# Kernel optimization log

Hardware: AMD Instinct MI355X
Metric: run time of the kernel (lower is better)

The kernel has to match this reference:

```python
import jax, jax.numpy as jnp
import numpy as np

B, S, D, H = 4, 1024, 1024, 16
DH = D // H  # head_dim = 64


def setup_inputs() -> dict:
    key = jax.random.key(0)
    kq, kk, kv, kl, kwq, kwk, kwv, kwo = jax.random.split(key, 8)
    query = jax.random.normal(kq, (B, S, D), dtype=jnp.float32)
    key_t = jax.random.normal(kk, (B, S, D), dtype=jnp.float32)
    value = jax.random.normal(kv, (B, S, D), dtype=jnp.float32)
    # padding: keys at positions >= valid length are padded (True)
    lengths = jax.random.randint(kl, (B,), S // 2, S + 1)
    key_padding_mask = jnp.arange(S)[None, :] >= lengths[:, None]  # [B,S] bool
    scale = 1.0 / np.sqrt(D)
    Wq = jax.random.normal(kwq, (D, D), dtype=jnp.float32) * scale
    Wk = jax.random.normal(kwk, (D, D), dtype=jnp.float32) * scale
    Wv = jax.random.normal(kwv, (D, D), dtype=jnp.float32) * scale
    Wo = jax.random.normal(kwo, (D, D), dtype=jnp.float32) * scale
    gamma = jnp.ones((H,), dtype=jnp.float32)
    return {"query": query, "key": key_t, "value": value,
            "key_padding_mask": key_padding_mask,
            "Wq": Wq, "Wk": Wk, "Wv": Wv, "Wo": Wo, "gamma": gamma}


def reference(query, key, value, key_padding_mask, Wq, Wk, Wv, Wo, gamma):
    # nn.Linear(x) = x @ W.T (bias=False)
    q = jnp.einsum('bsd,ed->bse', query, Wq).reshape(B, S, H, DH).transpose(0, 2, 1, 3)  # [B,H,S,Dh]
    k = jnp.einsum('bsd,ed->bse', key, Wk).reshape(B, S, H, DH).transpose(0, 2, 1, 3)
    v = jnp.einsum('bsd,ed->bse', value, Wv).reshape(B, S, H, DH).transpose(0, 2, 1, 3)
    scores = jnp.einsum('bhqd,bhkd->bhqk', q, k) / jnp.sqrt(jnp.float32(DH))
    pad = key_padding_mask[:, None, None, :]  # [B,1,1,S]
    scores = jnp.where(pad, -jnp.inf, scores)
    v = jnp.where(key_padding_mask[:, None, :, None], 0.0, v)
    attn = jax.nn.softmax(scores, axis=-1)  # dropout p=0 (eval) -> identity
    ws = jnp.einsum('bhqk,bhkd->bhqd', attn, v)
    ws = ws * gamma[None, :, None, None]  # per-head scale
    ws = ws.transpose(0, 2, 1, 3).reshape(B, S, D)
    return jnp.einsum('bsd,ed->bse', ws, Wo)
```

## Files before the change

### kernel.cpp

```cpp
#include <hip/hip_runtime.h>
#include <math.h>

#define S_LEN 1024
#define DMODEL 1024

typedef __attribute__((ext_vector_type(8))) short bf16x8;
typedef __attribute__((ext_vector_type(4))) short bf16x4;
typedef __attribute__((ext_vector_type(4))) float f32x4;

#define MFMA16(a, b, c) __builtin_amdgcn_mfma_f32_16x16x32_bf16(a, b, c, 0, 0, 0)

#define WP (1024u * 1024u)
#define XP (4u * 1024u * 1024u)

__device__ __forceinline__ unsigned short rne_bf16(float f) {
    unsigned u = __float_as_uint(f);
    u += 0x7FFFu + ((u >> 16) & 1u);
    return (unsigned short)(u >> 16);
}

__device__ __forceinline__ void split_rne(float f, unsigned short& h, unsigned short& l) {
    unsigned short hh = rne_bf16(f);
    float lf = f - __uint_as_float(((unsigned)hh) << 16);
    h = hh;
    l = rne_bf16(lf);
}

typedef const __attribute__((address_space(1))) unsigned int* gas_t;
typedef __attribute__((address_space(3))) unsigned int* las_t;
__device__ __forceinline__ void glds16(const void* g, void* l) {
    __builtin_amdgcn_global_load_lds((gas_t)g, (las_t)l, 16, 0, 0);
}

__global__ __launch_bounds__(256)
void convert_wx(const float* __restrict__ W0, const float* __restrict__ W1,
                const float* __restrict__ W2, const float* __restrict__ W3,
                const float* __restrict__ Xq, const float* __restrict__ Xk,
                const float* __restrict__ Xv,
                unsigned short* __restrict__ Wpl, unsigned short* __restrict__ Xbase) {
    int blk = blockIdx.x;
    if (blk < 4096) {
        const int which = blk >> 10;
        const float* W = which == 0 ? W0 : which == 1 ? W1 : which == 2 ? W2 : W3;
        int i = ((blk & 1023) * 256 + threadIdx.x) * 4;
        float4 f = *(const float4*)&W[i];
        if (which == 3) {
            unsigned short* hi = Wpl + 3 * WP;
            unsigned short* lo = Wpl + 4 * WP;
            bf16x4 h, l;
            unsigned short hh, ll;
            split_rne(f.x, hh, ll); h[0] = (short)hh; l[0] = (short)ll;
            split_rne(f.y, hh, ll); h[1] = (short)hh; l[1] = (short)ll;
            split_rne(f.z, hh, ll); h[2] = (short)hh; l[2] = (short)ll;
            split_rne(f.w, hh, ll); h[3] = (short)hh; l[3] = (short)ll;
            *(bf16x4*)&hi[i] = h;
            *(bf16x4*)&lo[i] = l;
        } else {
            unsigned short* hi = Wpl + (size_t)which * WP;
            bf16x4 h;
            h[0] = (short)rne_bf16(f.x);
            h[1] = (short)rne_bf16(f.y);
            h[2] = (short)rne_bf16(f.z);
            h[3] = (short)rne_bf16(f.w);
            *(bf16x4*)&hi[i] = h;
        }
    } else {
        blk -= 4096;
        const int which = blk >> 12;
        const float* X = which == 0 ? Xq : which == 1 ? Xk : Xv;
        unsigned short* Xr = Xbase + (size_t)which * XP;
        int i = ((blk & 4095) * 256 + threadIdx.x) * 4;
        float4 f = *(const float4*)&X[i];
        bf16x4 h;
        h[0] = (short)rne_bf16(f.x);
        h[1] = (short)rne_bf16(f.y);
        h[2] = (short)rne_bf16(f.z);
        h[3] = (short)rne_bf16(f.w);
        *(bf16x4*)&Xr[i] = h;
    }
}

__global__ __launch_bounds__(256)
void gemm_proj(const unsigned short* __restrict__ Xbase,
               const unsigned short* __restrict__ Wpl,
               unsigned short* __restrict__ Obase) {
    __shared__ unsigned short AS[128 * 32];
    __shared__ unsigned short BS[128 * 32];

    const int z = blockIdx.z;
    const unsigned short* A = Xbase + (size_t)z * XP;
    const unsigned short* B = Wpl + (size_t)z * WP;

    const int t = threadIdx.x, lane = t & 63, w = t >> 6;
    const int quad = lane >> 4, l15 = lane & 15;
    const int wr = w & 1, wc = w >> 1;
    const int rowBase = blockIdx.y * 128, colBase = blockIdx.x * 128;

    const unsigned short* gA[2];
    const unsigned short* gB[2];
    unsigned short* lA[2];
    unsigned short* lB[2];
    #pragma unroll
    for (int e = 0; e < 2; e++) {
        int row = w * 32 + e * 16 + (lane >> 2);
        int cg = (lane & 3) ^ ((row >> 1) & 3);
        gA[e] = A + (size_t)(rowBase + row) * 1024 + cg * 8;
        gB[e] = B + (size_t)(colBase + row) * 1024 + cg * 8;
        lA[e] = &AS[(w * 32 + e * 16) * 32];
        lB[e] = &BS[(w * 32 + e * 16) * 32];
    }

    int aAd[4], bAd[4];
    #pragma unroll
    for (int i = 0; i < 4; i++) {
        int ra = wr * 64 + i * 16 + l15;
        aAd[i] = ra * 32 + (quad ^ ((ra >> 1) & 3)) * 8;
        int rb = wc * 64 + i * 16 + l15;
        bAd[i] = rb * 32 + (quad ^ ((rb >> 1) & 3)) * 8;
    }

    f32x4 acc[4][4] = {};

    for (int kt = 0; kt < 32; kt++) {
        if (kt) __syncthreads();
        const int ko = kt * 32;
        glds16(gA[0] + ko, lA[0]);
        glds16(gA[1] + ko, lA[1]);
        glds16(gB[0] + ko, lB[0]);
        glds16(gB[1] + ko, lB[1]);
        __syncthreads();

        bf16x8 af[4], bfr[4];
        #pragma unroll
        for (int i = 0; i < 4; i++) af[i] = *(const bf16x8*)&AS[aAd[i]];
        #pragma unroll
        for (int j = 0; j < 4; j++) bfr[j] = *(const bf16x8*)&BS[bAd[j]];
        #pragma unroll
        for (int j = 0; j < 4; j++)
            #pragma unroll
            for (int i = 0; i < 4; i++)
                acc[i][j] = MFMA16(af[i], bfr[j], acc[i][j]);
    }

    unsigned short* O = Obase + (size_t)z * XP;
    #pragma unroll
    for (int i = 0; i < 4; i++)
        #pragma unroll
        for (int j = 0; j < 4; j++)
            #pragma unroll
            for (int r = 0; r < 4; r++) {
                int m = rowBase + wr * 64 + i * 16 + quad * 4 + r;
                int n = colBase + wc * 64 + j * 16 + l15;
                int bb = m >> 10, s = m & 1023, hh = n >> 6, dh = n & 63;
                size_t hb = ((size_t)(bb * 16 + hh)) << 16;
                unsigned short v = rne_bf16(acc[i][j][r]);
                if (z == 2) O[hb + (size_t)dh * 1024 + s] = v;
                else        O[hb + s * 64 + dh] = v;
            }
}

__global__ __launch_bounds__(256)
void gemm_out2(const unsigned short* __restrict__ A,
               const unsigned short* __restrict__ Bh, const unsigned short* __restrict__ Bl,
               float* __restrict__ Cf) {
    __shared__ unsigned short AS[128 * 32];
    __shared__ unsigned short BhS[64 * 32], BlS[64 * 32];

    const int t = threadIdx.x, lane = t & 63, w = t >> 6;
    const int quad = lane >> 4, l15 = lane & 15;
    const int wr = w & 1, wc = w >> 1;
    const int rowBase = blockIdx.y * 128, colBase = blockIdx.x * 64;

    const unsigned short* gA[2];
    unsigned short* lA[2];
    #pragma unroll
    for (int e = 0; e < 2; e++) {
        int row = w * 32 + e * 16 + (lane >> 2);
        int cg = (lane & 3) ^ ((row >> 1) & 3);
        gA[e] = A + (size_t)(rowBase + row) * 1024 + cg * 8;
        lA[e] = &AS[(w * 32 + e * 16) * 32];
    }
    const unsigned short *gBh, *gBl;
    unsigned short *lBh, *lBl;
    {
        int row = w * 16 + (lane >> 2);
        int cg = (lane & 3) ^ ((row >> 1) & 3);
        gBh = Bh + (size_t)(colBase + row) * 1024 + cg * 8;
        gBl = Bl + (size_t)(colBase + row) * 1024 + cg * 8;
        lBh = &BhS[(w * 16) * 32];
        lBl = &BlS[(w * 16) * 32];
    }

    int aAd[4], bAd[2];
    #pragma unroll
    for (int i = 0; i < 4; i++) {
        int ra = wr * 64 + i * 16 + l15;
        aAd[i] = ra * 32 + (quad ^ ((ra >> 1) & 3)) * 8;
    }
    #pragma unroll
    for (int j = 0; j < 2; j++) {
        int rb = wc * 32 + j * 16 + l15;
        bAd[j] = rb * 32 + (quad ^ ((rb >> 1) & 3)) * 8;
    }

    f32x4 acc[4][2] = {};

    for (int kt = 0; kt < 32; kt++) {
        if (kt) __syncthreads();
        const int ko = kt * 32;
        glds16(gA[0] + ko, lA[0]);
        glds16(gA[1] + ko, lA[1]);
        glds16(gBh + ko, lBh);
        glds16(gBl + ko, lBl);
        __syncthreads();

        bf16x8 af[4], bhf[2], blf[2];
        #pragma unroll
        for (int i = 0; i < 4; i++) af[i] = *(const bf16x8*)&AS[aAd[i]];
        #pragma unroll
        for (int j = 0; j < 2; j++) {
            bhf[j] = *(const bf16x8*)&BhS[bAd[j]];
            blf[j] = *(const bf16x8*)&BlS[bAd[j]];
        }
        #pragma unroll
        for (int j = 0; j < 2; j++)
            #pragma unroll
            for (int i = 0; i < 4; i++) {
                acc[i][j] = MFMA16(af[i], bhf[j], acc[i][j]);
                acc[i][j] = MFMA16(af[i], blf[j], acc[i][j]);
            }
    }

    #pragma unroll
    for (int i = 0; i < 4; i++)
        #pragma unroll
        for (int j = 0; j < 2; j++)
            #pragma unroll
            for (int r = 0; r < 4; r++) {
                int m = rowBase + wr * 64 + i * 16 + quad * 4 + r;
                int n = colBase + wc * 32 + j * 16 + l15;
                Cf[(size_t)m * 1024 + n] = acc[i][j][r];
            }
}

__global__ __launch_bounds__(256)
void attn_mfma(const unsigned short* __restrict__ Qr, const unsigned short* __restrict__ Kr,
               const unsigned short* __restrict__ Vt,
               const int* __restrict__ mask, const float* __restrict__ gamma,
               unsigned short* __restrict__ WSr) {
    __shared__ int maskS[1024];
    __shared__ unsigned short Ks[64 * 72];
    __shared__ unsigned short Vs[64 * 72];
    __shared__ unsigned short Ph[4 * 16 * 72];

    const int t = threadIdx.x, lane = t & 63, w = t >> 6;
    const int quad = lane >> 4, l15 = lane & 15;
    const int q0 = blockIdx.x * 64, h = blockIdx.y, b = blockIdx.z;
    const size_t hb = ((size_t)(b * 16 + h)) << 16;

    ((int4*)maskS)[t] = ((const int4*)(mask + b * 1024))[t];

    bf16x8 qhi[2];
    {
        const int qrow = q0 + w * 16 + l15;
        const size_t qb = hb + (size_t)qrow * 64 + quad * 8;
        qhi[0] = *(const bf16x8*)&Qr[qb];
        qhi[1] = *(const bf16x8*)&Qr[qb + 32];
    }

    f32x4 o[4] = {};
    float lsum[4] = {0.f, 0.f, 0.f, 0.f};

    __syncthreads();

    for (int jt = 0; jt < 16; jt++) {
        const int j0 = jt * 64;
        if (maskS[j0]) break;
        const bool partial = maskS[j0 + 63] != 0;
        __syncthreads();
        #pragma unroll
        for (int e = 0; e < 2; e++) {
            int lin = e * 256 + t;
            int c = lin & 7, row = lin >> 3;
            *(bf16x8*)&Ks[row * 72 + c * 8] =
                *(const bf16x8*)&Kr[hb + (size_t)(j0 + row) * 64 + c * 8];
            *(bf16x8*)&Vs[row * 72 + c * 8] =
                *(const bf16x8*)&Vt[hb + (size_t)row * 1024 + j0 + c * 8];
        }
        __syncthreads();

        f32x4 s4[4] = {};
        #pragma unroll
        for (int nj = 0; nj < 4; nj++) {
            int kr = (nj * 16 + l15) * 72 + quad * 8;
            #pragma unroll
            for (int kk = 0; kk < 2; kk++) {
                bf16x8 kv = *(const bf16x8*)&Ks[kr + kk * 32];
                s4[nj] = MFMA16(qhi[kk], kv, s4[nj]);
            }
        }

        if (partial) {
            #pragma unroll
            for (int nj = 0; nj < 4; nj++) {
                int mk = maskS[j0 + nj * 16 + l15];
                #pragma unroll
                for (int r = 0; r < 4; r++) {
                    float p = mk ? 0.f : __expf(s4[nj][r] * 0.125f);
                    lsum[r] += p;
                    Ph[(w * 16 + quad * 4 + r) * 72 + nj * 16 + l15] = rne_bf16(p);
                }
            }
        } else {
            #pragma unroll
            for (int nj = 0; nj < 4; nj++) {
                #pragma unroll
                for (int r = 0; r < 4; r++) {
                    float p = __expf(s4[nj][r] * 0.125f);
                    lsum[r] += p;
                    Ph[(w * 16 + quad * 4 + r) * 72 + nj * 16 + l15] = rne_bf16(p);
                }
            }
        }

        bf16x8 ph[2];
        #pragma unroll
        for (int ks = 0; ks < 2; ks++)
            ph[ks] = *(const bf16x8*)&Ph[(w * 16 + l15) * 72 + ks * 32 + quad * 8];
        #pragma unroll
        for (int dt = 0; dt < 4; dt++) {
            int vr = (dt * 16 + l15) * 72 + quad * 8;
            #pragma unroll
            for (int ks = 0; ks < 2; ks++) {
                bf16x8 vv = *(const bf16x8*)&Vs[vr + ks * 32];
                o[dt] = MFMA16(ph[ks], vv, o[dt]);
            }
        }
    }

    #pragma unroll
    for (int r = 0; r < 4; r++) {
        lsum[r] += __shfl_xor(lsum[r], 1);
        lsum[r] += __shfl_xor(lsum[r], 2);
        lsum[r] += __shfl_xor(lsum[r], 4);
        lsum[r] += __shfl_xor(lsum[r], 8);
    }

    const float g = gamma[h];
    #pragma unroll
    for (int r = 0; r < 4; r++) {
        const int qrow = q0 + w * 16 + quad * 4 + r;
        const float sc = g / lsum[r];
        const size_t base = ((size_t)b * 1024 + qrow) * 1024 + h * 64;
        #pragma unroll
        for (int dt = 0; dt < 4; dt++)
            WSr[base + dt * 16 + l15] = rne_bf16(o[dt][r] * sc);
    }
}

extern "C" void kernel_launch(void* const* d_in, const int* in_sizes, int n_in,
                              void* d_out, int out_size, void* d_ws, size_t ws_size,
                              hipStream_t stream) {
    const float* query = (const float*)d_in[0];
    const float* key   = (const float*)d_in[1];
    const float* value = (const float*)d_in[2];
    const int*   mask  = (const int*)d_in[3];
    const float* Wq    = (const float*)d_in[4];
    const float* Wk    = (const float*)d_in[5];
    const float* Wv    = (const float*)d_in[6];
    const float* Wo    = (const float*)d_in[7];
    const float* gamma = (const float*)d_in[8];
    float* out = (float*)d_out;

    unsigned short* u = (unsigned short*)d_ws;
    unsigned short* Xbase = u;
    unsigned short* Obase = u + 3 * XP;
    unsigned short* Wpl   = u + 6 * XP;
    unsigned short* WSr   = Xbase;
    unsigned short* Qr = Obase, *Kr = Obase + XP, *Vt = Obase + 2 * XP;
    unsigned short* Woh = Wpl + 3 * WP, *Wol = Wpl + 4 * WP;

    convert_wx<<<16384, 256, 0, stream>>>(Wq, Wk, Wv, Wo, query, key, value, Wpl, Xbase);

    gemm_proj<<<dim3(8, 32, 3), 256, 0, stream>>>(Xbase, Wpl, Obase);

    attn_mfma<<<dim3(16, 16, 4), 256, 0, stream>>>(Qr, Kr, Vt, mask, gamma, WSr);

    gemm_out2<<<dim3(16, 32), 256, 0, stream>>>(WSr, Woh, Wol, out);
}
```

Baseline: 211.9 us.

## Pre-swizzle operands into MFMA fragment layout and drop LDS staging in GEMMs

The conversion kernel and the attention epilogue now write bf16 operands in a tiled layout that matches the MFMA 16x16x32 fragment order. Each lane can then load its fragment straight from global memory with one contiguous 16-byte read. Both GEMMs lose their shared-memory staging and barriers and instead use register double-buffering of global loads. The output GEMM also grows to 128x128 tiles. This removes LDS traffic and synchronisation, but it relies on L2/cache reuse across waves instead of shared-memory reuse, and it raises register pressure.

```diff
diff --git a/kernel.cpp b/kernel.cpp
--- a/kernel.cpp
+++ b/kernel.cpp
@@ -5,7 +5,6 @@
 #define DMODEL 1024
 
 typedef __attribute__((ext_vector_type(8))) short bf16x8;
-typedef __attribute__((ext_vector_type(4))) short bf16x4;
 typedef __attribute__((ext_vector_type(4))) float f32x4;
 
 #define MFMA16(a, b, c) __builtin_amdgcn_mfma_f32_16x16x32_bf16(a, b, c, 0, 0, 0)
@@ -19,127 +18,110 @@
     return (unsigned short)(u >> 16);
 }
 
-__device__ __forceinline__ void split_rne(float f, unsigned short& h, unsigned short& l) {
-    unsigned short hh = rne_bf16(f);
-    float lf = f - __uint_as_float(((unsigned)hh) << 16);
-    h = hh;
-    l = rne_bf16(lf);
-}
-
-typedef const __attribute__((address_space(1))) unsigned int* gas_t;
-typedef __attribute__((address_space(3))) unsigned int* las_t;
-__device__ __forceinline__ void glds16(const void* g, void* l) {
-    __builtin_amdgcn_global_load_lds((gas_t)g, (las_t)l, 16, 0, 0);
-}
 
 __global__ __launch_bounds__(256)
-void convert_wx(const float* __restrict__ W0, const float* __restrict__ W1,
+void convert_sw(const float* __restrict__ W0, const float* __restrict__ W1,
                 const float* __restrict__ W2, const float* __restrict__ W3,
                 const float* __restrict__ Xq, const float* __restrict__ Xk,
                 const float* __restrict__ Xv,
-                unsigned short* __restrict__ Wpl, unsigned short* __restrict__ Xbase) {
-    int blk = blockIdx.x;
-    if (blk < 4096) {
-        const int which = blk >> 10;
-        const float* W = which == 0 ? W0 : which == 1 ? W1 : which == 2 ? W2 : W3;
-        int i = ((blk & 1023) * 256 + threadIdx.x) * 4;
-        float4 f = *(const float4*)&W[i];
-        if (which == 3) {
-            unsigned short* hi = Wpl + 3 * WP;
-            unsigned short* lo = Wpl + 4 * WP;
-            bf16x4 h, l;
-            unsigned short hh, ll;
-            split_rne(f.x, hh, ll); h[0] = (short)hh; l[0] = (short)ll;
-            split_rne(f.y, hh, ll); h[1] = (short)hh; l[1] = (short)ll;
-            split_rne(f.z, hh, ll); h[2] = (short)hh; l[2] = (short)ll;
-            split_rne(f.w, hh, ll); h[3] = (short)hh; l[3] = (short)ll;
-            *(bf16x4*)&hi[i] = h;
-            *(bf16x4*)&lo[i] = l;
-        } else {
-            unsigned short* hi = Wpl + (size_t)which * WP;
-            bf16x4 h;
-            h[0] = (short)rne_bf16(f.x);
-            h[1] = (short)rne_bf16(f.y);
-            h[2] = (short)rne_bf16(f.z);
-            h[3] = (short)rne_bf16(f.w);
-            *(bf16x4*)&hi[i] = h;
-        }
+                unsigned short* __restrict__ Wsw, unsigned short* __restrict__ Xsw) {
+    const int blk = blockIdx.x, t = threadIdx.x;
+    const float* S;
+    unsigned short* D;
+    unsigned short* D2 = nullptr;
+    int p;
+    if (blk < 256) {
+        const int which = blk >> 6;
+        p = blk & 63;
+        S = which == 0 ? W0 : which == 1 ? W1 : which == 2 ? W2 : W3;
+        if (which == 3) { D = Wsw + 3 * WP; D2 = Wsw + 4 * WP; }
+        else            { D = Wsw + (size_t)which * WP; }
     } else {
-        blk -= 4096;
-        const int which = blk >> 12;
-        const float* X = which == 0 ? Xq : which == 1 ? Xk : Xv;
-        unsigned short* Xr = Xbase + (size_t)which * XP;
-        int i = ((blk & 4095) * 256 + threadIdx.x) * 4;
-        float4 f = *(const float4*)&X[i];
-        bf16x4 h;
-        h[0] = (short)rne_bf16(f.x);
-        h[1] = (short)rne_bf16(f.y);
-        h[2] = (short)rne_bf16(f.z);
-        h[3] = (short)rne_bf16(f.w);
-        *(bf16x4*)&Xr[i] = h;
+        const int which = (blk - 256) >> 8;
+        p = (blk - 256) & 255;
+        S = which == 0 ? Xq : which == 1 ? Xk : Xv;
+        D = Xsw + (size_t)which * XP;
+    }
+    const int n15 = t & 15;
+    const size_t rowOff = (size_t)(p * 16 + n15) * 1024;
+    #pragma unroll
+    for (int e = 0; e < 8; e++) {
+        int kchunk = e * 16 + (t >> 4);
+        int k0 = kchunk * 8;
+        float4 f0 = *(const float4*)&S[rowOff + k0];
+        float4 f1 = *(const float4*)&S[rowOff + k0 + 4];
+        int kt = kchunk >> 2, kc = kchunk & 3;
+        size_t dst = ((size_t)(p * 32 + kt) * 64 + kc * 16 + n15) * 8;
+        float v[8] = {f0.x, f0.y, f0.z, f0.w, f1.x, f1.y, f1.z, f1.w};
+        bf16x8 h;
+        #pragma unroll
+        for (int i = 0; i < 8; i++) h[i] = (short)rne_bf16(v[i]);
+        *(bf16x8*)&D[dst] = h;
+        if (D2) {
+            bf16x8 l;
+            #pragma unroll
+            for (int i = 0; i < 8; i++) {
+                float lf = v[i] - __uint_as_float(((unsigned)(unsigned short)h[i]) << 16);
+                l[i] = (short)rne_bf16(lf);
+            }
+            *(bf16x8*)&D2[dst] = l;
+        }
     }
 }
 
 __global__ __launch_bounds__(256)
-void gemm_proj(const unsigned short* __restrict__ Xbase,
-               const unsigned short* __restrict__ Wpl,
+void gemm_proj(const unsigned short* __restrict__ Xsw,
+               const unsigned short* __restrict__ Wsw,
                unsigned short* __restrict__ Obase) {
-    __shared__ unsigned short AS[128 * 32];
-    __shared__ unsigned short BS[128 * 32];
-
     const int z = blockIdx.z;
-    const unsigned short* A = Xbase + (size_t)z * XP;
-    const unsigned short* B = Wpl + (size_t)z * WP;
+    const unsigned short* A = Xsw + (size_t)z * XP;
+    const unsigned short* B = Wsw + (size_t)z * WP;
 
     const int t = threadIdx.x, lane = t & 63, w = t >> 6;
     const int quad = lane >> 4, l15 = lane & 15;
     const int wr = w & 1, wc = w >> 1;
-    const int rowBase = blockIdx.y * 128, colBase = blockIdx.x * 128;
-
-    const unsigned short* gA[2];
-    const unsigned short* gB[2];
-    unsigned short* lA[2];
-    unsigned short* lB[2];
-    #pragma unroll
-    for (int e = 0; e < 2; e++) {
-        int row = w * 32 + e * 16 + (lane >> 2);
-        int cg = (lane & 3) ^ ((row >> 1) & 3);
-        gA[e] = A + (size_t)(rowBase + row) * 1024 + cg * 8;
-        gB[e] = B + (size_t)(colBase + row) * 1024 + cg * 8;
-        lA[e] = &AS[(w * 32 + e * 16) * 32];
-        lB[e] = &BS[(w * 32 + e * 16) * 32];
-    }
-
-    int aAd[4], bAd[4];
+    const int mt0 = blockIdx.y * 8 + wr * 4;
+    const int nt0 = blockIdx.x * 8 + wc * 4;
+
+    int aoff[4], boff[4];
     #pragma unroll
     for (int i = 0; i < 4; i++) {
-        int ra = wr * 64 + i * 16 + l15;
-        aAd[i] = ra * 32 + (quad ^ ((ra >> 1) & 3)) * 8;
-        int rb = wc * 64 + i * 16 + l15;
-        bAd[i] = rb * 32 + (quad ^ ((rb >> 1) & 3)) * 8;
+        aoff[i] = ((mt0 + i) * 32 * 64 + lane) * 8;
+        boff[i] = ((nt0 + i) * 32 * 64 + lane) * 8;
     }
 
     f32x4 acc[4][4] = {};
-
-    for (int kt = 0; kt < 32; kt++) {
-        if (kt) __syncthreads();
-        const int ko = kt * 32;
-        glds16(gA[0] + ko, lA[0]);
-        glds16(gA[1] + ko, lA[1]);
-        glds16(gB[0] + ko, lB[0]);
-        glds16(gB[1] + ko, lB[1]);
-        __syncthreads();
-
-        bf16x8 af[4], bfr[4];
-        #pragma unroll
-        for (int i = 0; i < 4; i++) af[i] = *(const bf16x8*)&AS[aAd[i]];
-        #pragma unroll
-        for (int j = 0; j < 4; j++) bfr[j] = *(const bf16x8*)&BS[bAd[j]];
+    bf16x8 a0[4], b0[4], a1[4], b1[4];
+
+    #pragma unroll
+    for (int i = 0; i < 4; i++) {
+        a0[i] = *(const bf16x8*)&A[aoff[i]];
+        b0[i] = *(const bf16x8*)&B[boff[i]];
+    }
+
+    for (int kt = 0; kt < 32; kt += 2) {
+        #pragma unroll
+        for (int i = 0; i < 4; i++) {
+            a1[i] = *(const bf16x8*)&A[aoff[i] + (kt + 1) * 512];
+            b1[i] = *(const bf16x8*)&B[boff[i] + (kt + 1) * 512];
+        }
         #pragma unroll
         for (int j = 0; j < 4; j++)
             #pragma unroll
             for (int i = 0; i < 4; i++)
-                acc[i][j] = MFMA16(af[i], bfr[j], acc[i][j]);
+                acc[i][j] = MFMA16(a0[i], b0[j], acc[i][j]);
+        if (kt + 2 < 32) {
+            #pragma unroll
+            for (int i = 0; i < 4; i++) {
+                a0[i] = *(const bf16x8*)&A[aoff[i] + (kt + 2) * 512];
+                b0[i] = *(const bf16x8*)&B[boff[i] + (kt + 2) * 512];
+            }
+        }
+        #pragma unroll
+        for (int j = 0; j < 4; j++)
+            #pragma unroll
+            for (int i = 0; i < 4; i++)
+                acc[i][j] = MFMA16(a1[i], b1[j], acc[i][j]);
     }
 
     unsigned short* O = Obase + (size_t)z * XP;
@@ -149,8 +131,8 @@
         for (int j = 0; j < 4; j++)
             #pragma unroll
             for (int r = 0; r < 4; r++) {
-                int m = rowBase + wr * 64 + i * 16 + quad * 4 + r;
-                int n = colBase + wc * 64 + j * 16 + l15;
+                int m = blockIdx.y * 128 + wr * 64 + i * 16 + quad * 4 + r;
+                int n = blockIdx.x * 128 + wc * 64 + j * 16 + l15;
                 int bb = m >> 10, s = m & 1023, hh = n >> 6, dh = n & 63;
                 size_t hb = ((size_t)(bb * 16 + hh)) << 16;
                 unsigned short v = rne_bf16(acc[i][j][r]);
@@ -163,82 +145,68 @@
 void gemm_out2(const unsigned short* __restrict__ A,
                const unsigned short* __restrict__ Bh, const unsigned short* __restrict__ Bl,
                float* __restrict__ Cf) {
-    __shared__ unsigned short AS[128 * 32];
-    __shared__ unsigned short BhS[64 * 32], BlS[64 * 32];
-
     const int t = threadIdx.x, lane = t & 63, w = t >> 6;
     const int quad = lane >> 4, l15 = lane & 15;
     const int wr = w & 1, wc = w >> 1;
-    const int rowBase = blockIdx.y * 128, colBase = blockIdx.x * 64;
-
-    const unsigned short* gA[2];
-    unsigned short* lA[2];
-    #pragma unroll
-    for (int e = 0; e < 2; e++) {
-        int row = w * 32 + e * 16 + (lane >> 2);
-        int cg = (lane & 3) ^ ((row >> 1) & 3);
-        gA[e] = A + (size_t)(rowBase + row) * 1024 + cg * 8;
-        lA[e] = &AS[(w * 32 + e * 16) * 32];
-    }
-    const unsigned short *gBh, *gBl;
-    unsigned short *lBh, *lBl;
-    {
-        int row = w * 16 + (lane >> 2);
-        int cg = (lane & 3) ^ ((row >> 1) & 3);
-        gBh = Bh + (size_t)(colBase + row) * 1024 + cg * 8;
-        gBl = Bl + (size_t)(colBase + row) * 1024 + cg * 8;
-        lBh = &BhS[(w * 16) * 32];
-        lBl = &BlS[(w * 16) * 32];
-    }
-
-    int aAd[4], bAd[2];
+    const int mt0 = blockIdx.y * 8 + wr * 4;
+    const int nt0 = blockIdx.x * 8 + wc * 4;
+
+    int aoff[4], boff[4];
     #pragma unroll
     for (int i = 0; i < 4; i++) {
-        int ra = wr * 64 + i * 16 + l15;
-        aAd[i] = ra * 32 + (quad ^ ((ra >> 1) & 3)) * 8;
-    }
-    #pragma unroll
-    for (int j = 0; j < 2; j++) {
-        int rb = wc * 32 + j * 16 + l15;
-        bAd[j] = rb * 32 + (quad ^ ((rb >> 1) & 3)) * 8;
-    }
-
-    f32x4 acc[4][2] = {};
-
-    for (int kt = 0; kt < 32; kt++) {
-        if (kt) __syncthreads();
-        const int ko = kt * 32;
-        glds16(gA[0] + ko, lA[0]);
-        glds16(gA[1] + ko, lA[1]);
-        glds16(gBh + ko, lBh);
-        glds16(gBl + ko, lBl);
-        __syncthreads();
-
-        bf16x8 af[4], bhf[2], blf[2];
-        #pragma unroll
-        for (int i = 0; i < 4; i++) af[i] = *(const bf16x8*)&AS[aAd[i]];
-        #pragma unroll
-        for (int j = 0; j < 2; j++) {
-            bhf[j] = *(const bf16x8*)&BhS[bAd[j]];
-            blf[j] = *(const bf16x8*)&BlS[bAd[j]];
-        }
-        #pragma unroll
-        for (int j = 0; j < 2; j++)
+        aoff[i] = ((mt0 + i) * 32 * 64 + lane) * 8;
+        boff[i] = ((nt0 + i) * 32 * 64 + lane) * 8;
+    }
+
+    f32x4 acc[4][4] = {};
+    bf16x8 a0[4], bh0[4], bl0[4], a1[4], bh1[4], bl1[4];
+
+    #pragma unroll
+    for (int i = 0; i < 4; i++) {
+        a0[i]  = *(const bf16x8*)&A [aoff[i]];
+        bh0[i] = *(const bf16x8*)&Bh[boff[i]];
+        bl0[i] = *(const bf16x8*)&Bl[boff[i]];
+    }
+
+    for (int kt = 0; kt < 32; kt += 2) {
+        #pragma unroll
+        for (int i = 0; i < 4; i++) {
+            a1[i]  = *(const bf16x8*)&A [aoff[i] + (kt + 1) * 512];
+            bh1[i] = *(const bf16x8*)&Bh[boff[i] + (kt + 1) * 512];
+            bl1[i] = *(const bf16x8*)&Bl[boff[i] + (kt + 1) * 512];
+        }
+        #pragma unroll
+        for (int j = 0; j < 4; j++)
             #pragma unroll
             for (int i = 0; i < 4; i++) {
-                acc[i][j] = MFMA16(af[i], bhf[j], acc[i][j]);
-                acc[i][j] = MFMA16(af[i], blf[j], acc[i][j]);
+                acc[i][j] = MFMA16(a0[i], bh0[j], acc[i][j]);
+                acc[i][j] = MFMA16(a0[i], bl0[j], acc[i][j]);
+            }
+        if (kt + 2 < 32) {
+            #pragma unroll
+            for (int i = 0; i < 4; i++) {
+                a0[i]  = *(const bf16x8*)&A [aoff[i] + (kt + 2) * 512];
+                bh0[i] = *(const bf16x8*)&Bh[boff[i] + (kt + 2) * 512];
+                bl0[i] = *(const bf16x8*)&Bl[boff[i] + (kt + 2) * 512];
+            }
+        }
+        #pragma unroll
+        for (int j = 0; j < 4; j++)
+            #pragma unroll
+            for (int i = 0; i < 4; i++) {
+                acc[i][j] = MFMA16(a1[i], bh1[j], acc[i][j]);
+                acc[i][j] = MFMA16(a1[i], bl1[j], acc[i][j]);
             }
     }
 
     #pragma unroll
     for (int i = 0; i < 4; i++)
         #pragma unroll
-        for (int j = 0; j < 2; j++)
+        for (int j = 0; j < 4; j++)
             #pragma unroll
             for (int r = 0; r < 4; r++) {
-                int m = rowBase + wr * 64 + i * 16 + quad * 4 + r;
-                int n = colBase + wc * 32 + j * 16 + l15;
+                int m = blockIdx.y * 128 + wr * 64 + i * 16 + quad * 4 + r;
+                int n = blockIdx.x * 128 + wc * 64 + j * 16 + l15;
                 Cf[(size_t)m * 1024 + n] = acc[i][j][r];
             }
 }
@@ -247,7 +215,7 @@
 void attn_mfma(const unsigned short* __restrict__ Qr, const unsigned short* __restrict__ Kr,
                const unsigned short* __restrict__ Vt,
                const int* __restrict__ mask, const float* __restrict__ gamma,
-               unsigned short* __restrict__ WSr) {
+               unsigned short* __restrict__ WSsw) {
     __shared__ int maskS[1024];
     __shared__ unsigned short Ks[64 * 72];
     __shared__ unsigned short Vs[64 * 72];
@@ -347,14 +315,18 @@
     }
 
     const float g = gamma[h];
+    const int mt = ((b * 1024 + q0) >> 4) + w;
     #pragma unroll
     for (int r = 0; r < 4; r++) {
-        const int qrow = q0 + w * 16 + quad * 4 + r;
+        const int m15 = quad * 4 + r;
         const float sc = g / lsum[r];
-        const size_t base = ((size_t)b * 1024 + qrow) * 1024 + h * 64;
-        #pragma unroll
-        for (int dt = 0; dt < 4; dt++)
-            WSr[base + dt * 16 + l15] = rne_bf16(o[dt][r] * sc);
+        #pragma unroll
+        for (int dt = 0; dt < 4; dt++) {
+            int kg = h * 64 + dt * 16 + l15;
+            int kt = kg >> 5, kc = (kg >> 3) & 3, j = kg & 7;
+            WSsw[((size_t)(mt * 32 + kt) * 64 + kc * 16 + m15) * 8 + j] =
+                rne_bf16(o[dt][r] * sc);
+        }
     }
 }
 
@@ -373,18 +345,18 @@
     float* out = (float*)d_out;
 
     unsigned short* u = (unsigned short*)d_ws;
-    unsigned short* Xbase = u;
+    unsigned short* Xsw  = u;
     unsigned short* Obase = u + 3 * XP;
-    unsigned short* Wpl   = u + 6 * XP;
-    unsigned short* WSr   = Xbase;
+    unsigned short* Wsw  = u + 6 * XP;
+    unsigned short* WSsw = Xsw;
     unsigned short* Qr = Obase, *Kr = Obase + XP, *Vt = Obase + 2 * XP;
-    unsigned short* Woh = Wpl + 3 * WP, *Wol = Wpl + 4 * WP;
-
-    convert_wx<<<16384, 256, 0, stream>>>(Wq, Wk, Wv, Wo, query, key, value, Wpl, Xbase);
-
-    gemm_proj<<<dim3(8, 32, 3), 256, 0, stream>>>(Xbase, Wpl, Obase);
-
-    attn_mfma<<<dim3(16, 16, 4), 256, 0, stream>>>(Qr, Kr, Vt, mask, gamma, WSr);
-
-    gemm_out2<<<dim3(16, 32), 256, 0, stream>>>(WSr, Woh, Wol, out);
-}
+    unsigned short* Woh = Wsw + 3 * WP, *Wol = Wsw + 4 * WP;
+
+    convert_sw<<<1024, 256, 0, stream>>>(Wq, Wk, Wv, Wo, query, key, value, Wsw, Xsw);
+
+    gemm_proj<<<dim3(8, 32, 3), 256, 0, stream>>>(Xsw, Wsw, Obase);
+
+    attn_mfma<<<dim3(16, 16, 4), 256, 0, stream>>>(Qr, Kr, Vt, mask, gamma, WSsw);
+
+    gemm_out2<<<dim3(8, 32), 256, 0, stream>>>(WSsw, Woh, Wol, out);
+}
```

Measured after the change: 238.9 us. 1.13x slower.
